# Performance work log

Measured on AMD Instinct MI355X. Metric: run time of the kernel, lower is better.

The kernel has to match this reference:

```python
import jax, jax.numpy as jnp
import numpy as np

# Static module configuration (matches init_kwargs)
NLAT, NLON = 256, 256
LMAX = 128            # max_degree
MMAX = 129            # nlon//2 + 1 == max_degree + 1
CIN, COUT, BATCH = 32, 32, 8
NUM_COEFFS = 2 * LMAX * MMAX  # real+imag flattened, = 33024


def _cc_quadrature(n):
    """Clenshaw-Curtis nodes (colatitudes incl. poles) and weights on [-1,1]."""
    N = n - 1
    tj = np.pi * np.arange(n) / N
    k = np.arange(1, N // 2 + 1)
    bk = np.where(2 * k == N, 1.0, 2.0)
    S = np.cos(2.0 * np.outer(tj, k)) @ (bk / (4.0 * k * k - 1.0))
    c = np.full(n, 2.0)
    c[0] = c[-1] = 1.0
    w = (c / N) * (1.0 - S)
    return tj, w


def _legpoly(mmax, lmax, t):
    """Orthonormal associated Legendre P_l^m(cos t) incl. 1/sqrt(4pi) and CS phase.
    Returns array [mmax, lmax, nlat]; entries with l < m are zero."""
    ct, st = np.cos(t), np.sin(t)
    p = np.zeros((mmax, lmax, t.shape[0]))
    p[0, 0] = 1.0 / np.sqrt(4.0 * np.pi)
    for m in range(1, min(mmax, lmax)):
        p[m, m] = -np.sqrt((2.0 * m + 1.0) / (2.0 * m)) * st * p[m - 1, m - 1]
    for m in range(min(mmax, lmax)):
        if m + 1 < lmax:
            p[m, m + 1] = np.sqrt(2.0 * m + 3.0) * ct * p[m, m]
    for m in range(mmax):
        for l in range(m + 2, lmax):
            a = np.sqrt((4.0 * l * l - 1.0) / (l * l - m * m))
            b = np.sqrt(((l - 1.0) ** 2 - m * m) / (4.0 * (l - 1.0) ** 2 - 1.0))
            p[m, l] = a * (ct * p[m, l - 1] - b * p[m, l - 2])
    return p


_T, _WQ = _cc_quadrature(NLAT)
_PCT_NP = _legpoly(MMAX, LMAX, _T)                 # synthesis Legendre matrix
_PCT = jnp.asarray(_PCT_NP, jnp.float32)           # [mmax, lmax, nlat]
_PCTW = jnp.asarray(_PCT_NP * _WQ[None, None, :], jnp.float32)  # analysis (quadrature weighted)


def setup_inputs() -> dict:
    key = jax.random.key(0)
    k1, k2 = jax.random.split(key)
    x = jax.random.normal(k1, (BATCH, CIN, NLAT, NLON), jnp.float32)
    scale = (1.0 / (CIN * COUT * NUM_COEFFS)) ** 0.5
    weight = scale * jax.random.normal(k2, (CIN, COUT, NUM_COEFFS), jnp.float32)
    return {"x": x, "weight": weight}


def reference(x, weight):
    B, C = x.shape[0], x.shape[1]
    # ---- forward real SHT (ortho norm, equiangular / Clenshaw-Curtis) ----
    # longitudinal rfft with 'forward' norm, scaled by 2*pi
    xh = (2.0 * np.pi / NLON) * jnp.fft.rfft(x, axis=-1)   # [B,C,nlat,nlon//2+1] complex
    xh = xh[..., :MMAX]
    re = jnp.einsum('bckm,mlk->bclm', jnp.real(xh), _PCTW)  # [B,C,lmax,mmax]
    im = jnp.einsum('bckm,mlk->bclm', jnp.imag(xh), _PCTW)
    spec = jnp.stack([re, im], axis=-1).reshape(B, C, NUM_COEFFS)
    # ---- spectral channel mixing: per-coefficient dense channel mix ----
    out = jnp.einsum('bix,iox->box', spec, weight)          # [B,Cout,NUM_COEFFS]
    out = out.reshape(B, COUT, LMAX, MMAX, 2)
    # ---- inverse real SHT ----
    rr = jnp.einsum('bolm,mlk->bokm', out[..., 0], _PCT)    # [B,Cout,nlat,mmax]
    ri = jnp.einsum('bolm,mlk->bokm', out[..., 1], _PCT)
    Xm = jax.lax.complex(rr, ri)                            # mmax == nlon//2+1
    y = jnp.fft.irfft(Xm, n=NLON, axis=-1) * NLON           # irfft norm='forward'
    return y
```

## Files before the change

kernel.cpp:

```cpp
#include <hip/hip_runtime.h>


typedef __attribute__((ext_vector_type(8))) short short8;
typedef __attribute__((ext_vector_type(4))) float f32x4;

__device__ __forceinline__ ushort bf16_rtn(float v) {
  uint u = __float_as_uint(v);
  return (ushort)((u + 0x7FFFu + ((u >> 16) & 1u)) >> 16);
}
__device__ __forceinline__ void split2(float v, ushort& h, ushort& l) {
  h = bf16_rtn(v);
  float hf = __uint_as_float(((uint)h) << 16);
  l = bf16_rtn(v - hf);
}
__device__ __forceinline__ void gl2lds16(const ushort* g, short* l) {
  __builtin_amdgcn_global_load_lds(
      (const __attribute__((address_space(1))) unsigned int*)g,
      (__attribute__((address_space(3))) unsigned int*)l, 16, 0, 0);
}

__global__ __launch_bounds__(256) void k_tables(
    ushort* __restrict__ Th, ushort* __restrict__ Tl,
    ushort* __restrict__ TiTh, ushort* __restrict__ TiTl,
    ushort* __restrict__ PWh, ushort* __restrict__ PWl,
    ushort* __restrict__ PTh, ushort* __restrict__ PTl) {
  const double PI = 3.14159265358979323846264338327950288;
  const int t = threadIdx.x;
  const int m = blockIdx.x;
  __shared__ double sCos[256];
  __shared__ double sCoef[128];
  __shared__ double sRatio[128];
  __shared__ double sA[128], sB[128];

  if (m == 128) {
    const double scale = 2.0 * PI / 256.0;
    sCos[t] = cos(scale * (double)t);
    __syncthreads();
    const int n = t;
    for (int ch = 0; ch < 8; ++ch) {
      uint th16[16], tl16[16];
#pragma unroll
      for (int j = 0; j < 16; ++j) {
        const int mm = ch * 16 + j;
        const int r = (mm * n) & 255;
        const double c = sCos[r];
        const double s = sCos[(r + 192) & 255];
        const double wm = (mm == 0) ? 1.0 : 2.0;
        ushort h, l;
        split2((float)(scale * c), h, l);  Th[(2*mm)*256+n]=h;   Tl[(2*mm)*256+n]=l;
        split2((float)(-scale * s), h, l); Th[(2*mm+1)*256+n]=h; Tl[(2*mm+1)*256+n]=l;
        ushort h2, l2b, h3, l3;
        split2((float)(wm * c), h2, l2b);
        split2((float)(-wm * s), h3, l3);
        th16[j] = (uint)h2 | ((uint)h3 << 16);
        tl16[j] = (uint)l2b | ((uint)l3 << 16);
      }
      const int base = n * 256 + ch * 32;
#pragma unroll
      for (int q4 = 0; q4 < 4; ++q4) {
        *(uint4*)(TiTh + base + q4 * 8) = make_uint4(th16[4*q4], th16[4*q4+1], th16[4*q4+2], th16[4*q4+3]);
        *(uint4*)(TiTl + base + q4 * 8) = make_uint4(tl16[4*q4], tl16[4*q4+1], tl16[4*q4+2], tl16[4*q4+3]);
      }
    }
    return;
  }

  const double scale255 = 2.0 * PI / 255.0;
  if (t < 255) sCos[t] = cos(scale255 * (double)t);
  if (t >= 1 && t < 128) {
    const double dt = (double)t;
    sCoef[t]  = 2.0 / (4.0 * dt * dt - 1.0);
    sRatio[t] = (2.0 * dt + 1.0) / (2.0 * dt);
    if (t >= m + 2) {
      const double dl = dt, dm = (double)m;
      sA[t] = sqrt((4.0*dl*dl - 1.0) / (dl*dl - dm*dm));
      sB[t] = sqrt(((dl-1.0)*(dl-1.0) - dm*dm) / (4.0*(dl-1.0)*(dl-1.0) - 1.0));
    }
  }
  __syncthreads();

  const int k = t;
  const double tj = PI * (double)k / 255.0;
  double ssum = 0.0;
  {
    int r = 0;
    for (int kk = 1; kk <= 127; ++kk) {
      r += k; if (r >= 255) r -= 255;
      ssum += sCoef[kk] * sCos[r];
    }
  }
  const double cj = (k == 0 || k == 255) ? 1.0 : 2.0;
  const double wq = cj / 255.0 * (1.0 - ssum);
  const double ct = cos(tj), st = sin(tj);
  double prod = 1.0, stp = 1.0;
  for (int mm = 1; mm <= m; ++mm) { prod *= sRatio[mm]; stp *= -st; }
  const double pmm = (1.0 / sqrt(4.0 * PI)) * sqrt(prod) * stp;
  const double sq2m3 = sqrt(2.0 * (double)m + 3.0);

  const size_t pwB = (size_t)m * 32768;
  const size_t ptB = (size_t)m * 32768 + (size_t)k * 128;
  double plm1 = 0.0, plm2 = 0.0;
  for (int lc0 = 0; lc0 < 128; lc0 += 16) {
    uint hq[8], lq[8];
#pragma unroll
    for (int j = 0; j < 16; ++j) {
      const int l = lc0 + j;
      double val;
      if (l < m)           val = 0.0;
      else if (l == m)     val = pmm;
      else if (l == m + 1) val = sq2m3 * ct * pmm;
      else                 val = sA[l] * (ct * plm1 - sB[l] * plm2);
      plm2 = plm1; plm1 = val;
      ushort h, lo; split2((float)val, h, lo);
      if ((j & 1) == 0) { hq[j>>1] = (uint)h; lq[j>>1] = (uint)lo; }
      else              { hq[j>>1] |= ((uint)h) << 16; lq[j>>1] |= ((uint)lo) << 16; }
      ushort hw, lw; split2((float)(val * wq), hw, lw);
      PWh[pwB + (size_t)l * 256 + k] = hw;
      PWl[pwB + (size_t)l * 256 + k] = lw;
    }
    *(uint4*)(PTh + ptB + lc0)     = make_uint4(hq[0], hq[1], hq[2], hq[3]);
    *(uint4*)(PTh + ptB + lc0 + 8) = make_uint4(hq[4], hq[5], hq[6], hq[7]);
    *(uint4*)(PTl + ptB + lc0)     = make_uint4(lq[0], lq[1], lq[2], lq[3]);
    *(uint4*)(PTl + ptB + lc0 + 8) = make_uint4(lq[4], lq[5], lq[6], lq[7]);
  }
}

template<int AM, int BM, int CM>
__global__ __launch_bounds__(256) void mfma_gemm(
    const ushort* __restrict__ Ah, const ushort* __restrict__ Al, const float* __restrict__ Af,
    const ushort* __restrict__ Bh, const ushort* __restrict__ Bl, const float* __restrict__ Bf,
    float* __restrict__ C, ushort* __restrict__ Ch, ushort* __restrict__ Cl,
    int lda, int ldb, int ldc, int K,
    long aZ, int aShift, long bZ, int bShift, long cZ, int cColOff,
    int kFromZ, int mSkipFromZ)
{
  __shared__ __align__(16) short sAh[128*32];
  __shared__ __align__(16) short sAl[128*32];
  __shared__ __align__(16) short sBh[128*32];
  __shared__ __align__(16) short sBl[128*32];
  const int z = blockIdx.z;
  const long aOff = ((long)(z >> aShift)) * aZ;
  const long bOff = ((long)(z >> bShift)) * bZ;
  const long cOff = (long)z * cZ;
  const int i0 = blockIdx.y * 128;
  const int j0 = blockIdx.x * 128;
  const int t = threadIdx.x;
  const int lane = t & 63, w = t >> 6;
  const int wy = w >> 1, wx = w & 1;
  const int il = lane & 15, q = lane >> 4;
  const int kstart = kFromZ ? ((z >> 1) & ~31) : 0;
  const int nsk = mSkipFromZ ? ((z >> 1) >> 4) : 0;
  const int grow0 = w * 32 + (lane >> 2);
  const int gchunk0 = (lane & 3) ^ ((lane >> 3) & 3);
  const int cq = q ^ ((il >> 1) & 3);

  f32x4 acc[4][4];
#pragma unroll
  for (int a = 0; a < 4; ++a)
#pragma unroll
    for (int b = 0; b < 4; ++b) acc[a][b] = (f32x4){0.f, 0.f, 0.f, 0.f};

  for (int k0 = kstart; k0 < K; k0 += 32) {
    __syncthreads();
    if constexpr (AM == 0) {
#pragma unroll
      for (int inst = 0; inst < 2; ++inst) {
        const int r = grow0 + inst * 16;
        const size_t g = (size_t)aOff + (size_t)(i0 + r) * lda + k0 + gchunk0 * 8;
        short* dA = &sAh[(w * 32 + inst * 16) * 32];
        short* dAl = &sAl[(w * 32 + inst * 16) * 32];
        gl2lds16(Ah + g, dA);
        gl2lds16(Al + g, dAl);
      }
    } else {
      const int kk0 = 8*w + 2*q;
      const int cbase = kk0 >> 3, koff = kk0 & 7;
      const float* s0 = Af + aOff + (size_t)(k0 + kk0) * lda + i0 + il;
      const float* s1 = s0 + lda;
#pragma unroll
      for (int c = 0; c < 8; ++c) {
        float v0 = s0[c*16], v1 = s1[c*16];
        ushort h0,l0,h1,l1; split2(v0,h0,l0); split2(v1,h1,l1);
        const int row = il + 16*c;
        const int idx = row*32 + ((cbase ^ ((row>>1)&3)) << 3) + koff;
        *(uint*)&sAh[idx] = (uint)h0 | ((uint)h1 << 16);
        *(uint*)&sAl[idx] = (uint)l0 | ((uint)l1 << 16);
      }
    }
    if constexpr (BM == 0) {
#pragma unroll
      for (int inst = 0; inst < 2; ++inst) {
        const int r = grow0 + inst * 16;
        const size_t g = (size_t)bOff + (size_t)(j0 + r) * ldb + k0 + gchunk0 * 8;
        short* dB = &sBh[(w * 32 + inst * 16) * 32];
        short* dBl = &sBl[(w * 32 + inst * 16) * 32];
        gl2lds16(Bh + g, dB);
        gl2lds16(Bl + g, dBl);
      }
    } else {
      const int rr = t >> 1, ks = (t & 1) * 16;
      const int rsw = (rr >> 1) & 3;
      const float* src = Bf + bOff + (size_t)(j0 + rr) * ldb + k0 + ks;
#pragma unroll
      for (int jj = 0; jj < 4; ++jj) {
        float4 f = *(const float4*)(src + 4*jj);
        ushort h0,l0,h1,l1,h2,l2,h3,l3;
        split2(f.x,h0,l0); split2(f.y,h1,l1); split2(f.z,h2,l2); split2(f.w,h3,l3);
        const int pos = ks + 4*jj;
        const int idx = rr*32 + ((((pos >> 3) ^ rsw)) << 3) + (pos & 7);
        *(ushort4*)&sBh[idx] = make_ushort4(h0,h1,h2,h3);
        *(ushort4*)&sBl[idx] = make_ushort4(l0,l1,l2,l3);
      }
    }
    __syncthreads();
    short8 afh[4], afl[4];
#pragma unroll
    for (int mi = 0; mi < 4; ++mi) {
      if (wy*4 + mi >= nsk) {
        const int row = wy*64 + mi*16 + il;
        afh[mi] = *(const short8*)&sAh[row*32 + cq*8];
        afl[mi] = *(const short8*)&sAl[row*32 + cq*8];
      }
    }
#pragma unroll
    for (int nj = 0; nj < 4; ++nj) {
      const int row = wx*64 + nj*16 + il;
      short8 bfh = *(const short8*)&sBh[row*32 + cq*8];
      short8 bfl = *(const short8*)&sBl[row*32 + cq*8];
#pragma unroll
      for (int mi = 0; mi < 4; ++mi) {
        if (wy*4 + mi >= nsk) {
          acc[mi][nj] = __builtin_amdgcn_mfma_f32_16x16x32_bf16(afh[mi], bfh, acc[mi][nj], 0, 0, 0);
          acc[mi][nj] = __builtin_amdgcn_mfma_f32_16x16x32_bf16(afh[mi], bfl, acc[mi][nj], 0, 0, 0);
          acc[mi][nj] = __builtin_amdgcn_mfma_f32_16x16x32_bf16(afl[mi], bfh, acc[mi][nj], 0, 0, 0);
        }
      }
    }
  }
#pragma unroll
  for (int mi = 0; mi < 4; ++mi)
#pragma unroll
    for (int nj = 0; nj < 4; ++nj)
#pragma unroll
      for (int r = 0; r < 4; ++r) {
        const long gi = i0 + wy*64 + mi*16 + q*4 + r;
        const long gj = j0 + wx*64 + nj*16 + il;
        if constexpr (CM == 0) {
          C[cOff + gi*ldc + cColOff + gj] = acc[mi][nj][r];
        } else {
          ushort h, lo; split2(acc[mi][nj][r], h, lo);
          const size_t idx = (size_t)(cOff + gi*ldc + cColOff + gj);
          Ch[idx] = h; Cl[idx] = lo;
        }
      }
}

__global__ __launch_bounds__(256) void k_stagec(const float* __restrict__ spec,
                                                const float* __restrict__ w,
                                                float* __restrict__ outb) {
  const int cb = blockIdx.x, l = blockIdx.y;
  if (cb * 16 > l) return;
  __shared__ float s_spec[32 * 257];
  __shared__ float s_w[256 * 33];
  const int t = threadIdx.x;
  const int c = t & 31, og = t >> 5;
  const size_t x0 = 258u * l + cb * 32;
  for (int cc = 0; cc < 32; ++cc)
    s_spec[cc * 257 + t] = spec[(size_t)(cb * 32 + cc) * 32768 + l * 256 + t];
  float acc[8][4] = {{0.f}};
  const int lr = t >> 4;
  const int lq = (t & 15) * 2;
  for (int isub = 0; isub < 4; ++isub) {
    __syncthreads();
    for (int pass = 0; pass < 16; ++pass) {
      const int rho = pass * 16 + lr;
      const int io = (isub * 8 + (rho >> 5)) * 32 + (rho & 31);
      const float2 wv = *(const float2*)&w[(size_t)io * 33024 + x0 + lq];
      s_w[rho * 33 + lq]     = wv.x;
      s_w[rho * 33 + lq + 1] = wv.y;
    }
    __syncthreads();
#pragma unroll
    for (int idp = 0; idp < 4; ++idp) {
      const int i0 = isub * 8 + idp * 2;
      const int r0 = idp * 64;
      float2 sv[8];
#pragma unroll
      for (int b = 0; b < 8; ++b)
        sv[b] = *(const float2*)&s_spec[c * 257 + b * 32 + i0];
      float wv0[4], wv1[4];
#pragma unroll
      for (int od = 0; od < 4; ++od) {
        wv0[od] = s_w[(r0 + og * 4 + od) * 33 + c];
        wv1[od] = s_w[(r0 + 32 + og * 4 + od) * 33 + c];
      }
#pragma unroll
      for (int b = 0; b < 8; ++b)
#pragma unroll
        for (int od = 0; od < 4; ++od)
          acc[b][od] = fmaf(sv[b].x, wv0[od], fmaf(sv[b].y, wv1[od], acc[b][od]));
    }
  }
  __syncthreads();
#pragma unroll
  for (int b = 0; b < 8; ++b)
#pragma unroll
    for (int od = 0; od < 4; ++od)
      s_w[c * 257 + b * 32 + og * 4 + od] = acc[b][od];
  __syncthreads();
  for (int cc = 0; cc < 32; ++cc)
    outb[(size_t)(cb * 32 + cc) * 32768 + l * 256 + t] = s_w[cc * 257 + t];
}

extern "C" void kernel_launch(void* const* d_in, const int* in_sizes, int n_in,
                              void* d_out, int out_size, void* d_ws, size_t ws_size,
                              hipStream_t stream) {
  const float* x = (const float*)d_in[0];
  const float* w = (const float*)d_in[1];
  float* y = (float*)d_out;
  char* ws = (char*)d_ws;

  ushort* Th   = (ushort*)(ws + 0);
  ushort* Tl   = (ushort*)(ws + 131072);
  ushort* TiTh = (ushort*)(ws + 262144);
  ushort* TiTl = (ushort*)(ws + 393216);
  ushort* PWh  = (ushort*)(ws + 524288);
  ushort* PWl  = (ushort*)(ws + 8912896);
  ushort* PTh  = (ushort*)(ws + 17301504);
  ushort* PTl  = (ushort*)(ws + 25690112);
  ushort* XHh  = (ushort*)(ws + 34078720);
  ushort* XHl  = (ushort*)(ws + 67633152);
  float* XM    = (float*)(ws + 34078720);
  float* spec  = (float*)(ws + 101187584);
  float* outb  = spec;

  k_tables<<<dim3(129), dim3(256), 0, stream>>>(Th, Tl, TiTh, TiTl, PWh, PWl, PTh, PTl);

  mfma_gemm<0,1,1><<<dim3(512, 2, 1), dim3(256), 0, stream>>>(
      Th, Tl, nullptr, nullptr, nullptr, x, nullptr, XHh, XHl,
      256, 256, 65536, 256, 0L, 0, 0L, 0, 0L, 0, 0, 0);

  mfma_gemm<0,0,0><<<dim3(2, 1, 256), dim3(256), 0, stream>>>(
      PWh, PWl, nullptr, XHh, XHl, nullptr, spec, nullptr, nullptr,
      256, 256, 256, 256, 32768L, 1, 65536L, 0, 32768L, 0, 0, 1);

  k_stagec<<<dim3(8, 128), dim3(256), 0, stream>>>(spec, w, outb);

  mfma_gemm<2,0,0><<<dim3(2, 2, 256), dim3(256), 0, stream>>>(
      nullptr, nullptr, outb, PTh, PTl, nullptr, XM, nullptr, nullptr,
      256, 128, 256, 128, 32768L, 0, 32768L, 1, 65536L, 0, 1, 0);

  mfma_gemm<2,0,0><<<dim3(2, 512, 1), dim3(256), 0, stream>>>(
      nullptr, nullptr, XM, TiTh, TiTl, nullptr, y, nullptr, nullptr,
      65536, 256, 256, 256, 0L, 0, 0L, 0, 0L, 0, 0, 0);
}
```

Measured before the change: 410.2 us.

## Pre-split intermediates into packed bf16 hi/lo and reorder z-blocks for balance

Producers of the mixed spectrum and of the Legendre-synthesis output now write each value as a packed 32-bit word holding its bf16 high and low halves. The consuming GEMMs (new AM==3 path) just unpack bits when staging into LDS instead of re-splitting floats in the inner loop. A ZB template flag remaps blockIdx.z so heavy and light triangular-skip slices are interleaved in dispatch order, improving load balance. The packed split happens once per element at the producer rather than per tile load, which removes ALU work from the hot loops at no change in memory traffic.

```diff
diff --git a/kernel.cpp b/kernel.cpp
--- a/kernel.cpp
+++ b/kernel.cpp
@@ -125,7 +125,7 @@
   }
 }
 
-template<int AM, int BM, int CM>
+template<int AM, int BM, int CM, int ZB>
 __global__ __launch_bounds__(256) void mfma_gemm(
     const ushort* __restrict__ Ah, const ushort* __restrict__ Al, const float* __restrict__ Af,
     const ushort* __restrict__ Bh, const ushort* __restrict__ Bl, const float* __restrict__ Bf,
@@ -138,7 +138,8 @@
   __shared__ __align__(16) short sAl[128*32];
   __shared__ __align__(16) short sBh[128*32];
   __shared__ __align__(16) short sBl[128*32];
-  const int z = blockIdx.z;
+  const int zraw = blockIdx.z;
+  const int z = ZB ? ((zraw < 128) ? zraw : 383 - zraw) : zraw;
   const long aOff = ((long)(z >> aShift)) * aZ;
   const long bOff = ((long)(z >> bShift)) * bZ;
   const long cOff = (long)z * cZ;
@@ -172,7 +173,7 @@
         gl2lds16(Ah + g, dA);
         gl2lds16(Al + g, dAl);
       }
-    } else {
+    } else if constexpr (AM == 2) {
       const int kk0 = 8*w + 2*q;
       const int cbase = kk0 >> 3, koff = kk0 & 7;
       const float* s0 = Af + aOff + (size_t)(k0 + kk0) * lda + i0 + il;
@@ -185,6 +186,20 @@
         const int idx = row*32 + ((cbase ^ ((row>>1)&3)) << 3) + koff;
         *(uint*)&sAh[idx] = (uint)h0 | ((uint)h1 << 16);
         *(uint*)&sAl[idx] = (uint)l0 | ((uint)l1 << 16);
+      }
+    } else {
+      const int kk0 = 8*w + 2*q;
+      const int cbase = kk0 >> 3, koff = kk0 & 7;
+      const float* s0 = Af + aOff + (size_t)(k0 + kk0) * lda + i0 + il;
+      const float* s1 = s0 + lda;
+#pragma unroll
+      for (int c = 0; c < 8; ++c) {
+        const uint v0 = __float_as_uint(s0[c*16]);
+        const uint v1 = __float_as_uint(s1[c*16]);
+        const int row = il + 16*c;
+        const int idx = row*32 + ((cbase ^ ((row>>1)&3)) << 3) + koff;
+        *(uint*)&sAh[idx] = (v0 >> 16) | (v1 & 0xFFFF0000u);
+        *(uint*)&sAl[idx] = (v0 & 0xFFFFu) | (v1 << 16);
       }
     }
     if constexpr (BM == 0) {
@@ -247,17 +262,20 @@
         const long gj = j0 + wx*64 + nj*16 + il;
         if constexpr (CM == 0) {
           C[cOff + gi*ldc + cColOff + gj] = acc[mi][nj][r];
-        } else {
+        } else if constexpr (CM == 1) {
           ushort h, lo; split2(acc[mi][nj][r], h, lo);
           const size_t idx = (size_t)(cOff + gi*ldc + cColOff + gj);
           Ch[idx] = h; Cl[idx] = lo;
+        } else {
+          ushort h, lo; split2(acc[mi][nj][r], h, lo);
+          ((uint*)C)[cOff + gi*ldc + cColOff + gj] = ((uint)h << 16) | lo;
         }
       }
 }
 
 __global__ __launch_bounds__(256) void k_stagec(const float* __restrict__ spec,
                                                 const float* __restrict__ w,
-                                                float* __restrict__ outb) {
+                                                uint* __restrict__ outb) {
   const int cb = blockIdx.x, l = blockIdx.y;
   if (cb * 16 > l) return;
   __shared__ float s_spec[32 * 257];
@@ -308,8 +326,11 @@
     for (int od = 0; od < 4; ++od)
       s_w[c * 257 + b * 32 + og * 4 + od] = acc[b][od];
   __syncthreads();
-  for (int cc = 0; cc < 32; ++cc)
-    outb[(size_t)(cb * 32 + cc) * 32768 + l * 256 + t] = s_w[cc * 257 + t];
+  for (int cc = 0; cc < 32; ++cc) {
+    const float v = s_w[cc * 257 + t];
+    ushort h, lo; split2(v, h, lo);
+    outb[(size_t)(cb * 32 + cc) * 32768 + l * 256 + t] = ((uint)h << 16) | lo;
+  }
 }
 
 extern "C" void kernel_launch(void* const* d_in, const int* in_sizes, int n_in,
@@ -332,25 +353,25 @@
   ushort* XHl  = (ushort*)(ws + 67633152);
   float* XM    = (float*)(ws + 34078720);
   float* spec  = (float*)(ws + 101187584);
-  float* outb  = spec;
+  uint* outb   = (uint*)spec;
 
   k_tables<<<dim3(129), dim3(256), 0, stream>>>(Th, Tl, TiTh, TiTl, PWh, PWl, PTh, PTl);
 
-  mfma_gemm<0,1,1><<<dim3(512, 2, 1), dim3(256), 0, stream>>>(
+  mfma_gemm<0,1,1,0><<<dim3(512, 2, 1), dim3(256), 0, stream>>>(
       Th, Tl, nullptr, nullptr, nullptr, x, nullptr, XHh, XHl,
       256, 256, 65536, 256, 0L, 0, 0L, 0, 0L, 0, 0, 0);
 
-  mfma_gemm<0,0,0><<<dim3(2, 1, 256), dim3(256), 0, stream>>>(
+  mfma_gemm<0,0,0,1><<<dim3(2, 1, 256), dim3(256), 0, stream>>>(
       PWh, PWl, nullptr, XHh, XHl, nullptr, spec, nullptr, nullptr,
       256, 256, 256, 256, 32768L, 1, 65536L, 0, 32768L, 0, 0, 1);
 
   k_stagec<<<dim3(8, 128), dim3(256), 0, stream>>>(spec, w, outb);
 
-  mfma_gemm<2,0,0><<<dim3(2, 2, 256), dim3(256), 0, stream>>>(
-      nullptr, nullptr, outb, PTh, PTl, nullptr, XM, nullptr, nullptr,
+  mfma_gemm<3,0,2,1><<<dim3(2, 2, 256), dim3(256), 0, stream>>>(
+      nullptr, nullptr, (const float*)outb, PTh, PTl, nullptr, XM, nullptr, nullptr,
       256, 128, 256, 128, 32768L, 0, 32768L, 1, 65536L, 0, 1, 0);
 
-  mfma_gemm<2,0,0><<<dim3(2, 512, 1), dim3(256), 0, stream>>>(
+  mfma_gemm<3,0,0,0><<<dim3(2, 512, 1), dim3(256), 0, stream>>>(
       nullptr, nullptr, XM, TiTh, TiTl, nullptr, y, nullptr, nullptr,
       65536, 256, 256, 256, 0L, 0, 0L, 0, 0L, 0, 0, 0);
 }
```

After: 414.8 us. About the same (+1.1%).
